# Optimization experiments

Measured on AMD Instinct MI355X. Metric: run time of the kernel, lower is better.

Reference implementation:

```python
import jax, jax.numpy as jnp
import numpy as np

PROP_TIME = 8  # matches init_kwargs prop_time


def _patches(x, dil):
    # x: [B,1,H,W] -> [B,9,H,W]; 'same' padding with the given dilation,
    # matching torch.nn.functional.unfold(kernel_size=3, dilation=dil, padding=dil).
    return jax.lax.conv_general_dilated_patches(
        x,
        filter_shape=(3, 3),
        window_strides=(1, 1),
        padding=[(dil, dil), (dil, dil)],
        rhs_dilation=(dil, dil),
    )


def setup_inputs() -> dict:
    key = jax.random.key(0)
    k1, k2, k3, k4 = jax.random.split(key, 4)
    B, H, W = 4, 352, 1216
    guided1 = jax.random.normal(k1, (B, 9, H, W), dtype=jnp.float32)
    guided2 = jax.random.normal(k2, (B, 9, H, W), dtype=jnp.float32)
    fuse = jax.random.uniform(k3, (B, 2, H, W), dtype=jnp.float32)
    x = jax.random.normal(k4, (B, 1, H, W), dtype=jnp.float32)
    return {"guided1": guided1, "guided2": guided2, "fuse": fuse, "x": x}


def reference(guided1, guided2, fuse, x):
    # softmax over the 9 kernel taps -> spatially varying normalized kernels
    kern1 = jax.nn.softmax(guided1, axis=1)  # [B,9,H,W]
    kern2 = jax.nn.softmax(guided2, axis=1)  # [B,9,H,W]
    f1 = fuse[:, 0:1]  # [B,1,H,W]
    f2 = fuse[:, 1:2]
    for _ in range(PROP_TIME):
        p1 = _patches(x, 1)  # [B,9,H,W]
        p2 = _patches(x, 2)
        o1 = jnp.sum(p1 * kern1, axis=1, keepdims=True)  # [B,1,H,W]
        o2 = jnp.sum(p2 * kern2, axis=1, keepdims=True)
        x = o1 * f1 + o2 * f2
    return x
```

## Files before the change

### kernel.cpp

```cpp
#include <hip/hip_runtime.h>

#define HH 352
#define WW 1216
#define NB 4
#define HWSZ (HH * WW)
#define WQ (WW / 4)
#define NQ (NB * HH * WQ)

typedef _Float16 half4 __attribute__((ext_vector_type(4)));
typedef _Float16 half8 __attribute__((ext_vector_type(8)));


__global__ __launch_bounds__(256, 4) void softmax_premul_kernel(
    const float* __restrict__ g1, const float* __restrict__ g2,
    const float* __restrict__ fuse, _Float16* __restrict__ ko) {
    int q = blockIdx.x * 256 + threadIdx.x;
    if (q >= NQ) return;
    int b   = q / (HH * WQ);
    int rem = q - b * (HH * WQ);
    long gbase = (long)b * 9 * HWSZ + (long)rem * 4;
    long fbase = (long)b * 2 * HWSZ + (long)rem * 4;

    float4 f1 = *(const float4*)(fuse + fbase);
    float4 f2 = *(const float4*)(fuse + fbase + HWSZ);

    half4 h1[9];
    {
        float e[9][4];
        float s0 = 0.f, s1 = 0.f, s2 = 0.f, s3 = 0.f;
#pragma unroll
        for (int k = 0; k < 9; k++) {
            float4 t = *(const float4*)(g1 + gbase + (long)k * HWSZ);
            e[k][0] = __expf(t.x); e[k][1] = __expf(t.y);
            e[k][2] = __expf(t.z); e[k][3] = __expf(t.w);
            s0 += e[k][0]; s1 += e[k][1]; s2 += e[k][2]; s3 += e[k][3];
        }
        float r0 = f1.x / s0, r1 = f1.y / s1, r2 = f1.z / s2, r3 = f1.w / s3;
#pragma unroll
        for (int k = 0; k < 9; k++) {
            h1[k][0] = (_Float16)(e[k][0] * r0);
            h1[k][1] = (_Float16)(e[k][1] * r1);
            h1[k][2] = (_Float16)(e[k][2] * r2);
            h1[k][3] = (_Float16)(e[k][3] * r3);
        }
    }
    {
        float e[9][4];
        float s0 = 0.f, s1 = 0.f, s2 = 0.f, s3 = 0.f;
#pragma unroll
        for (int k = 0; k < 9; k++) {
            float4 t = *(const float4*)(g2 + gbase + (long)k * HWSZ);
            e[k][0] = __expf(t.x); e[k][1] = __expf(t.y);
            e[k][2] = __expf(t.z); e[k][3] = __expf(t.w);
            s0 += e[k][0]; s1 += e[k][1]; s2 += e[k][2]; s3 += e[k][3];
        }
        float r0 = f2.x / s0, r1 = f2.y / s1, r2 = f2.z / s2, r3 = f2.w / s3;
        long obase = (long)b * 9 * HWSZ * 2 + (long)rem * 8;
#pragma unroll
        for (int k = 0; k < 9; k++) {
            half8 t;
            t[0] = h1[k][0]; t[1] = (_Float16)(e[k][0] * r0);
            t[2] = h1[k][1]; t[3] = (_Float16)(e[k][1] * r1);
            t[4] = h1[k][2]; t[5] = (_Float16)(e[k][2] * r2);
            t[6] = h1[k][3]; t[7] = (_Float16)(e[k][3] * r3);
            *(half8*)(ko + obase + (long)k * HWSZ * 2) = t;
        }
    }
}

#define TW 64
#define TH 4
#define LW (TW + 2)
#define LROWS (TH + 4)
#define LSTRIDE (LW * 4)
#define TILES_W ((WQ + TW - 1) / TW)
#define TILES_H (HH / TH)

__global__ __launch_bounds__(256, 4) void prop_kernel(
    const _Float16* __restrict__ kk,
    const float* __restrict__ xin, float* __restrict__ xout) {
    __shared__ float xs[LROWS][LSTRIDE];

    int tid = threadIdx.x;
    int bidx = blockIdx.x;
    int tX = bidx % TILES_W;
    int r1 = bidx / TILES_W;
    int tY = r1 % TILES_H;
    int b  = r1 / TILES_H;
    int q0 = tX * TW;
    int h0 = tY * TH;

    const float* xb = xin + (long)b * HWSZ;

#pragma unroll
    for (int i = tid; i < LROWS * LW; i += 256) {
        int row = i / LW;
        int qc  = i - row * LW;
        int h   = h0 - 2 + row;
        int qg  = q0 - 1 + qc;
        float4 v = make_float4(0.f, 0.f, 0.f, 0.f);
        if (h >= 0 && h < HH && qg >= 0 && qg < WQ)
            v = *(const float4*)(xb + (long)h * WW + qg * 4);
        *(float4*)&xs[row][qc * 4] = v;
    }
    __syncthreads();

    int tx = tid & (TW - 1);
    int ty = tid >> 6;
    int qa = q0 + tx;
    if (qa >= WQ) return;

    int h = h0 + ty;
    long p0 = (long)h * WW + qa * 4;
    long kbase = ((long)b * 9 * HWSZ + p0) * 2;

    half8 kv[9];
#pragma unroll
    for (int k = 0; k < 9; k++)
        kv[k] = *(const half8*)(kk + kbase + (long)k * HWSZ * 2);

    float rb[5][8];
#pragma unroll
    for (int r = 0; r < 5; r++) {
        const float* p = &xs[ty + r][4 * tx + 2];
        float2 a = *(const float2*)(p);
        float4 m = *(const float4*)(p + 2);
        float2 z = *(const float2*)(p + 6);
        rb[r][0] = a.x; rb[r][1] = a.y;
        rb[r][2] = m.x; rb[r][3] = m.y; rb[r][4] = m.z; rb[r][5] = m.w;
        rb[r][6] = z.x; rb[r][7] = z.y;
    }

    float o[4] = {0.f, 0.f, 0.f, 0.f};
#pragma unroll
    for (int ky = 0; ky < 3; ky++) {
#pragma unroll
        for (int kx = 0; kx < 3; kx++) {
            int k = ky * 3 + kx;
#pragma unroll
            for (int j = 0; j < 4; j++) {
                o[j] = fmaf((float)kv[k][2 * j],     rb[ky + 1][j + 1 + kx], o[j]);
                o[j] = fmaf((float)kv[k][2 * j + 1], rb[2 * ky][j + 2 * kx], o[j]);
            }
        }
    }

    float4 res = make_float4(o[0], o[1], o[2], o[3]);
    *(float4*)(xout + (long)b * HWSZ + p0) = res;
}

extern "C" void kernel_launch(void* const* d_in, const int* in_sizes, int n_in,
                              void* d_out, int out_size, void* d_ws, size_t ws_size,
                              hipStream_t stream) {
    const float* g1   = (const float*)d_in[0];
    const float* g2   = (const float*)d_in[1];
    const float* fuse = (const float*)d_in[2];
    const float* x    = (const float*)d_in[3];
    float* out = (float*)d_out;

    _Float16* kk = (_Float16*)d_ws;
    float* bufA  = (float*)(kk + (size_t)NB * 9 * HWSZ * 2);

    int sm_blocks = (NQ + 255) / 256;
    softmax_premul_kernel<<<sm_blocks, 256, 0, stream>>>(g1, g2, fuse, kk);

    int pr_blocks = NB * TILES_H * TILES_W;
    prop_kernel<<<pr_blocks, 256, 0, stream>>>(kk, x,    bufA);
    prop_kernel<<<pr_blocks, 256, 0, stream>>>(kk, bufA, out);
    prop_kernel<<<pr_blocks, 256, 0, stream>>>(kk, out,  bufA);
    prop_kernel<<<pr_blocks, 256, 0, stream>>>(kk, bufA, out);
    prop_kernel<<<pr_blocks, 256, 0, stream>>>(kk, out,  bufA);
    prop_kernel<<<pr_blocks, 256, 0, stream>>>(kk, bufA, out);
    prop_kernel<<<pr_blocks, 256, 0, stream>>>(kk, out,  bufA);
    prop_kernel<<<pr_blocks, 256, 0, stream>>>(kk, bufA, out);
}
```

Measured before the change: 266.4 us.

## Fuse two propagation steps per launch with halo recompute in shared memory

Each prop launch now performs two propagation iterations: it loads a wider x halo tile, computes the intermediate step over an extended region into shared memory, then computes the final step for the interior tile. This halves the number of launches and the global round-trips of x, at the cost of redundant halo computation and extra kernel-weight loads for halo pixels. The softmax kernel is also reorganized to issue all 18 loads up front, with a lower occupancy hint.

```diff
diff --git a/kernel.cpp b/kernel.cpp
--- a/kernel.cpp
+++ b/kernel.cpp
@@ -4,14 +4,13 @@
 #define WW 1216
 #define NB 4
 #define HWSZ (HH * WW)
-#define WQ (WW / 4)
+#define WQ 304
 #define NQ (NB * HH * WQ)
 
-typedef _Float16 half4 __attribute__((ext_vector_type(4)));
 typedef _Float16 half8 __attribute__((ext_vector_type(8)));
 
 
-__global__ __launch_bounds__(256, 4) void softmax_premul_kernel(
+__global__ __launch_bounds__(256, 2) void softmax_premul_kernel(
     const float* __restrict__ g1, const float* __restrict__ g2,
     const float* __restrict__ fuse, _Float16* __restrict__ ko) {
     int q = blockIdx.x * 256 + threadIdx.x;
@@ -21,132 +20,166 @@
     long gbase = (long)b * 9 * HWSZ + (long)rem * 4;
     long fbase = (long)b * 2 * HWSZ + (long)rem * 4;
 
+    float4 t[18];
+#pragma unroll
+    for (int k = 0; k < 9; k++) t[k]     = *(const float4*)(g1 + gbase + (long)k * HWSZ);
+#pragma unroll
+    for (int k = 0; k < 9; k++) t[9 + k] = *(const float4*)(g2 + gbase + (long)k * HWSZ);
     float4 f1 = *(const float4*)(fuse + fbase);
     float4 f2 = *(const float4*)(fuse + fbase + HWSZ);
 
-    half4 h1[9];
-    {
-        float e[9][4];
-        float s0 = 0.f, s1 = 0.f, s2 = 0.f, s3 = 0.f;
-#pragma unroll
-        for (int k = 0; k < 9; k++) {
-            float4 t = *(const float4*)(g1 + gbase + (long)k * HWSZ);
-            e[k][0] = __expf(t.x); e[k][1] = __expf(t.y);
-            e[k][2] = __expf(t.z); e[k][3] = __expf(t.w);
-            s0 += e[k][0]; s1 += e[k][1]; s2 += e[k][2]; s3 += e[k][3];
-        }
-        float r0 = f1.x / s0, r1 = f1.y / s1, r2 = f1.z / s2, r3 = f1.w / s3;
-#pragma unroll
-        for (int k = 0; k < 9; k++) {
-            h1[k][0] = (_Float16)(e[k][0] * r0);
-            h1[k][1] = (_Float16)(e[k][1] * r1);
-            h1[k][2] = (_Float16)(e[k][2] * r2);
-            h1[k][3] = (_Float16)(e[k][3] * r3);
-        }
-    }
-    {
-        float e[9][4];
-        float s0 = 0.f, s1 = 0.f, s2 = 0.f, s3 = 0.f;
-#pragma unroll
-        for (int k = 0; k < 9; k++) {
-            float4 t = *(const float4*)(g2 + gbase + (long)k * HWSZ);
-            e[k][0] = __expf(t.x); e[k][1] = __expf(t.y);
-            e[k][2] = __expf(t.z); e[k][3] = __expf(t.w);
-            s0 += e[k][0]; s1 += e[k][1]; s2 += e[k][2]; s3 += e[k][3];
-        }
-        float r0 = f2.x / s0, r1 = f2.y / s1, r2 = f2.z / s2, r3 = f2.w / s3;
-        long obase = (long)b * 9 * HWSZ * 2 + (long)rem * 8;
-#pragma unroll
-        for (int k = 0; k < 9; k++) {
-            half8 t;
-            t[0] = h1[k][0]; t[1] = (_Float16)(e[k][0] * r0);
-            t[2] = h1[k][1]; t[3] = (_Float16)(e[k][1] * r1);
-            t[4] = h1[k][2]; t[5] = (_Float16)(e[k][2] * r2);
-            t[6] = h1[k][3]; t[7] = (_Float16)(e[k][3] * r3);
-            *(half8*)(ko + obase + (long)k * HWSZ * 2) = t;
-        }
+    float s1[4] = {0.f, 0.f, 0.f, 0.f}, s2[4] = {0.f, 0.f, 0.f, 0.f};
+#pragma unroll
+    for (int k = 0; k < 9; k++) {
+        t[k].x = __expf(t[k].x); s1[0] += t[k].x;
+        t[k].y = __expf(t[k].y); s1[1] += t[k].y;
+        t[k].z = __expf(t[k].z); s1[2] += t[k].z;
+        t[k].w = __expf(t[k].w); s1[3] += t[k].w;
+    }
+#pragma unroll
+    for (int k = 9; k < 18; k++) {
+        t[k].x = __expf(t[k].x); s2[0] += t[k].x;
+        t[k].y = __expf(t[k].y); s2[1] += t[k].y;
+        t[k].z = __expf(t[k].z); s2[2] += t[k].z;
+        t[k].w = __expf(t[k].w); s2[3] += t[k].w;
+    }
+    float r1[4], r2[4];
+    r1[0] = f1.x / s1[0]; r1[1] = f1.y / s1[1]; r1[2] = f1.z / s1[2]; r1[3] = f1.w / s1[3];
+    r2[0] = f2.x / s2[0]; r2[1] = f2.y / s2[1]; r2[2] = f2.z / s2[2]; r2[3] = f2.w / s2[3];
+
+    long obase = ((long)b * 9 * HWSZ + (long)rem * 4) * 2;
+#pragma unroll
+    for (int k = 0; k < 9; k++) {
+        half8 o;
+        o[0] = (_Float16)(t[k].x * r1[0]); o[1] = (_Float16)(t[9 + k].x * r2[0]);
+        o[2] = (_Float16)(t[k].y * r1[1]); o[3] = (_Float16)(t[9 + k].y * r2[1]);
+        o[4] = (_Float16)(t[k].z * r1[2]); o[5] = (_Float16)(t[9 + k].z * r2[2]);
+        o[6] = (_Float16)(t[k].w * r1[3]); o[7] = (_Float16)(t[9 + k].w * r2[3]);
+        *(half8*)(ko + obase + (long)k * HWSZ * 2) = o;
     }
 }
 
-#define TW 64
-#define TH 4
-#define LW (TW + 2)
-#define LROWS (TH + 4)
-#define LSTRIDE (LW * 4)
-#define TILES_W ((WQ + TW - 1) / TW)
-#define TILES_H (HH / TH)
-
-__global__ __launch_bounds__(256, 4) void prop_kernel(
+#define CTH 8
+#define CTQ 76
+#define R1H 12
+#define R1Q 78
+#define X0H 16
+#define X0Q 80
+#define NREG (R1H * R1Q)
+
+__global__ __launch_bounds__(512, 2) void prop2_kernel(
     const _Float16* __restrict__ kk,
     const float* __restrict__ xin, float* __restrict__ xout) {
-    __shared__ float xs[LROWS][LSTRIDE];
-
-    int tid = threadIdx.x;
+    __shared__ float x0s[X0H][X0Q * 4];
+    __shared__ float x1s[R1H][R1Q * 4];
+
+    int tid  = threadIdx.x;
     int bidx = blockIdx.x;
-    int tX = bidx % TILES_W;
-    int r1 = bidx / TILES_W;
-    int tY = r1 % TILES_H;
-    int b  = r1 / TILES_H;
-    int q0 = tX * TW;
-    int h0 = tY * TH;
-
+    int tX = bidx & 3;
+    int rr = bidx >> 2;
+    int tY = rr % 44;
+    int b  = rr / 44;
+    int q0 = tX * CTQ;
+    int h0 = tY * CTH;
     const float* xb = xin + (long)b * HWSZ;
 
-#pragma unroll
-    for (int i = tid; i < LROWS * LW; i += 256) {
-        int row = i / LW;
-        int qc  = i - row * LW;
-        int h   = h0 - 2 + row;
-        int qg  = q0 - 1 + qc;
+    half8 kv[2][9];
+    int own_r[2], own_c[2];
+    bool own_v[2];
+#pragma unroll
+    for (int o = 0; o < 2; o++) {
+        int idx = tid + o * 512;
+        bool active = idx < NREG;
+        int r = idx / R1Q;
+        int c = idx - r * R1Q;
+        own_r[o] = r; own_c[o] = c;
+        int h  = h0 - 2 + r;
+        int qg = q0 - 1 + c;
+        bool valid = active && (h >= 0) && (h < HH) && (qg >= 0) && (qg < WQ);
+        own_v[o] = active;
+        long kb = ((long)b * 9 * HWSZ + (long)h * WW + qg * 4) * 2;
+#pragma unroll
+        for (int k = 0; k < 9; k++) {
+            half8 z = {};
+            kv[o][k] = valid ? *(const half8*)(kk + kb + (long)k * HWSZ * 2) : z;
+        }
+    }
+
+    for (int i = tid; i < X0H * X0Q; i += 512) {
+        int r = i / X0Q;
+        int c = i - r * X0Q;
+        int h  = h0 - 4 + r;
+        int qg = q0 - 2 + c;
         float4 v = make_float4(0.f, 0.f, 0.f, 0.f);
         if (h >= 0 && h < HH && qg >= 0 && qg < WQ)
             v = *(const float4*)(xb + (long)h * WW + qg * 4);
-        *(float4*)&xs[row][qc * 4] = v;
+        *(float4*)&x0s[r][c * 4] = v;
     }
     __syncthreads();
 
-    int tx = tid & (TW - 1);
-    int ty = tid >> 6;
-    int qa = q0 + tx;
-    if (qa >= WQ) return;
-
-    int h = h0 + ty;
-    long p0 = (long)h * WW + qa * 4;
-    long kbase = ((long)b * 9 * HWSZ + p0) * 2;
-
-    half8 kv[9];
-#pragma unroll
-    for (int k = 0; k < 9; k++)
-        kv[k] = *(const half8*)(kk + kbase + (long)k * HWSZ * 2);
-
-    float rb[5][8];
-#pragma unroll
-    for (int r = 0; r < 5; r++) {
-        const float* p = &xs[ty + r][4 * tx + 2];
-        float2 a = *(const float2*)(p);
-        float4 m = *(const float4*)(p + 2);
-        float2 z = *(const float2*)(p + 6);
-        rb[r][0] = a.x; rb[r][1] = a.y;
-        rb[r][2] = m.x; rb[r][3] = m.y; rb[r][4] = m.z; rb[r][5] = m.w;
-        rb[r][6] = z.x; rb[r][7] = z.y;
-    }
-
-    float o[4] = {0.f, 0.f, 0.f, 0.f};
-#pragma unroll
-    for (int ky = 0; ky < 3; ky++) {
-#pragma unroll
-        for (int kx = 0; kx < 3; kx++) {
-            int k = ky * 3 + kx;
-#pragma unroll
-            for (int j = 0; j < 4; j++) {
-                o[j] = fmaf((float)kv[k][2 * j],     rb[ky + 1][j + 1 + kx], o[j]);
-                o[j] = fmaf((float)kv[k][2 * j + 1], rb[2 * ky][j + 2 * kx], o[j]);
+#pragma unroll
+    for (int o = 0; o < 2; o++) {
+        if (!own_v[o]) continue;
+        int r = own_r[o], c = own_c[o];
+        float rb[5][8];
+#pragma unroll
+        for (int y = 0; y < 5; y++) {
+            const float* p = &x0s[r + y][4 * c + 2];
+            float2 a = *(const float2*)(p);
+            float4 m = *(const float4*)(p + 2);
+            float2 z = *(const float2*)(p + 6);
+            rb[y][0] = a.x; rb[y][1] = a.y;
+            rb[y][2] = m.x; rb[y][3] = m.y; rb[y][4] = m.z; rb[y][5] = m.w;
+            rb[y][6] = z.x; rb[y][7] = z.y;
+        }
+        float ov[4] = {0.f, 0.f, 0.f, 0.f};
+#pragma unroll
+        for (int ky = 0; ky < 3; ky++)
+#pragma unroll
+            for (int kx = 0; kx < 3; kx++) {
+                int k = ky * 3 + kx;
+#pragma unroll
+                for (int j = 0; j < 4; j++) {
+                    ov[j] = fmaf((float)kv[o][k][2 * j],     rb[ky + 1][j + 1 + kx], ov[j]);
+                    ov[j] = fmaf((float)kv[o][k][2 * j + 1], rb[2 * ky][j + 2 * kx], ov[j]);
+                }
             }
+        *(float4*)&x1s[r][c * 4] = make_float4(ov[0], ov[1], ov[2], ov[3]);
+    }
+    __syncthreads();
+
+#pragma unroll
+    for (int o = 0; o < 2; o++) {
+        int r = own_r[o], c = own_c[o];
+        if (!own_v[o] || r < 2 || r >= 10 || c < 1 || c >= 77) continue;
+        float rb[5][8];
+#pragma unroll
+        for (int y = 0; y < 5; y++) {
+            const float* p = &x1s[r - 2 + y][4 * c - 2];
+            float2 a = *(const float2*)(p);
+            float4 m = *(const float4*)(p + 2);
+            float2 z = *(const float2*)(p + 6);
+            rb[y][0] = a.x; rb[y][1] = a.y;
+            rb[y][2] = m.x; rb[y][3] = m.y; rb[y][4] = m.z; rb[y][5] = m.w;
+            rb[y][6] = z.x; rb[y][7] = z.y;
         }
-    }
-
-    float4 res = make_float4(o[0], o[1], o[2], o[3]);
-    *(float4*)(xout + (long)b * HWSZ + p0) = res;
+        float ov[4] = {0.f, 0.f, 0.f, 0.f};
+#pragma unroll
+        for (int ky = 0; ky < 3; ky++)
+#pragma unroll
+            for (int kx = 0; kx < 3; kx++) {
+                int k = ky * 3 + kx;
+#pragma unroll
+                for (int j = 0; j < 4; j++) {
+                    ov[j] = fmaf((float)kv[o][k][2 * j],     rb[ky + 1][j + 1 + kx], ov[j]);
+                    ov[j] = fmaf((float)kv[o][k][2 * j + 1], rb[2 * ky][j + 2 * kx], ov[j]);
+                }
+            }
+        int h  = h0 - 2 + r;
+        int qg = q0 - 1 + c;
+        *(float4*)(xout + (long)b * HWSZ + (long)h * WW + qg * 4) =
+            make_float4(ov[0], ov[1], ov[2], ov[3]);
+    }
 }
 
 extern "C" void kernel_launch(void* const* d_in, const int* in_sizes, int n_in,
@@ -164,13 +197,9 @@
     int sm_blocks = (NQ + 255) / 256;
     softmax_premul_kernel<<<sm_blocks, 256, 0, stream>>>(g1, g2, fuse, kk);
 
-    int pr_blocks = NB * TILES_H * TILES_W;
-    prop_kernel<<<pr_blocks, 256, 0, stream>>>(kk, x,    bufA);
-    prop_kernel<<<pr_blocks, 256, 0, stream>>>(kk, bufA, out);
-    prop_kernel<<<pr_blocks, 256, 0, stream>>>(kk, out,  bufA);
-    prop_kernel<<<pr_blocks, 256, 0, stream>>>(kk, bufA, out);
-    prop_kernel<<<pr_blocks, 256, 0, stream>>>(kk, out,  bufA);
-    prop_kernel<<<pr_blocks, 256, 0, stream>>>(kk, bufA, out);
-    prop_kernel<<<pr_blocks, 256, 0, stream>>>(kk, out,  bufA);
-    prop_kernel<<<pr_blocks, 256, 0, stream>>>(kk, bufA, out);
+    int pr_blocks = NB * 44 * 4;
+    prop2_kernel<<<pr_blocks, 512, 0, stream>>>(kk, x,    bufA);
+    prop2_kernel<<<pr_blocks, 512, 0, stream>>>(kk, bufA, out);
+    prop2_kernel<<<pr_blocks, 512, 0, stream>>>(kk, out,  bufA);
+    prop2_kernel<<<pr_blocks, 512, 0, stream>>>(kk, bufA, out);
 }
```

Measured after the change: 276.9 us. 1.04x slower.

## Fuse first propagation step into softmax kernel and store intermediates in fp16

Applied to the files above, without the earlier changes.

Folds the first propagation iteration into the softmax/premultiply kernel, which reads x directly from global memory and reuses the freshly computed kernel weights still held in registers. This removes one launch and one full pass over the fp16 kernel-weight buffer. Intermediate x buffers are also stored as fp16 rather than fp32, halving their read and write traffic; only the last step writes fp32. The trade-off is extra rounding error in x over the seven fp16 round trips, plus higher register pressure in the fused kernel.

```diff
diff --git a/kernel.cpp b/kernel.cpp
--- a/kernel.cpp
+++ b/kernel.cpp
@@ -4,82 +4,112 @@
 #define WW 1216
 #define NB 4
 #define HWSZ (HH * WW)
-#define WQ (WW / 4)
-#define NQ (NB * HH * WQ)
+#define WQ 304
+#define BHQ (HH * WQ)
+#define NQ (NB * BHQ)
 
 typedef _Float16 half4 __attribute__((ext_vector_type(4)));
 typedef _Float16 half8 __attribute__((ext_vector_type(8)));
 
 
-__global__ __launch_bounds__(256, 4) void softmax_premul_kernel(
+__global__ __launch_bounds__(256, 4) void softmax_prop1_kernel(
     const float* __restrict__ g1, const float* __restrict__ g2,
-    const float* __restrict__ fuse, _Float16* __restrict__ ko) {
+    const float* __restrict__ fuse, const float* __restrict__ x0,
+    _Float16* __restrict__ kk, _Float16* __restrict__ x1) {
     int q = blockIdx.x * 256 + threadIdx.x;
     if (q >= NQ) return;
-    int b   = q / (HH * WQ);
-    int rem = q - b * (HH * WQ);
+    int b   = q / BHQ;
+    int rem = q - b * BHQ;
+    int h   = rem / WQ;
+    int wq  = rem - h * WQ;
+    int w0  = wq * 4;
     long gbase = (long)b * 9 * HWSZ + (long)rem * 4;
     long fbase = (long)b * 2 * HWSZ + (long)rem * 4;
 
+    float4 t[18];
+#pragma unroll
+    for (int k = 0; k < 9; k++) t[k]     = *(const float4*)(g1 + gbase + (long)k * HWSZ);
+#pragma unroll
+    for (int k = 0; k < 9; k++) t[9 + k] = *(const float4*)(g2 + gbase + (long)k * HWSZ);
     float4 f1 = *(const float4*)(fuse + fbase);
     float4 f2 = *(const float4*)(fuse + fbase + HWSZ);
 
-    half4 h1[9];
-    {
-        float e[9][4];
-        float s0 = 0.f, s1 = 0.f, s2 = 0.f, s3 = 0.f;
-#pragma unroll
-        for (int k = 0; k < 9; k++) {
-            float4 t = *(const float4*)(g1 + gbase + (long)k * HWSZ);
-            e[k][0] = __expf(t.x); e[k][1] = __expf(t.y);
-            e[k][2] = __expf(t.z); e[k][3] = __expf(t.w);
-            s0 += e[k][0]; s1 += e[k][1]; s2 += e[k][2]; s3 += e[k][3];
+    float s1[4] = {0.f, 0.f, 0.f, 0.f}, s2[4] = {0.f, 0.f, 0.f, 0.f};
+#pragma unroll
+    for (int k = 0; k < 9; k++) {
+        t[k].x = __expf(t[k].x); s1[0] += t[k].x;
+        t[k].y = __expf(t[k].y); s1[1] += t[k].y;
+        t[k].z = __expf(t[k].z); s1[2] += t[k].z;
+        t[k].w = __expf(t[k].w); s1[3] += t[k].w;
+    }
+#pragma unroll
+    for (int k = 9; k < 18; k++) {
+        t[k].x = __expf(t[k].x); s2[0] += t[k].x;
+        t[k].y = __expf(t[k].y); s2[1] += t[k].y;
+        t[k].z = __expf(t[k].z); s2[2] += t[k].z;
+        t[k].w = __expf(t[k].w); s2[3] += t[k].w;
+    }
+    float r1[4], r2[4];
+    r1[0] = f1.x / s1[0]; r1[1] = f1.y / s1[1]; r1[2] = f1.z / s1[2]; r1[3] = f1.w / s1[3];
+    r2[0] = f2.x / s2[0]; r2[1] = f2.y / s2[1]; r2[2] = f2.z / s2[2]; r2[3] = f2.w / s2[3];
+
+    long obase = gbase * 2;
+    half8 kv[9];
+#pragma unroll
+    for (int k = 0; k < 9; k++) {
+        half8 o;
+        o[0] = (_Float16)(t[k].x * r1[0]); o[1] = (_Float16)(t[9 + k].x * r2[0]);
+        o[2] = (_Float16)(t[k].y * r1[1]); o[3] = (_Float16)(t[9 + k].y * r2[1]);
+        o[4] = (_Float16)(t[k].z * r1[2]); o[5] = (_Float16)(t[9 + k].z * r2[2]);
+        o[6] = (_Float16)(t[k].w * r1[3]); o[7] = (_Float16)(t[9 + k].w * r2[3]);
+        kv[k] = o;
+        *(half8*)(kk + obase + (long)k * HWSZ * 2) = o;
+    }
+
+    const float* xb = x0 + (long)b * HWSZ;
+    float rb[5][8];
+#pragma unroll
+    for (int r = 0; r < 5; r++) {
+        int hh = h - 2 + r;
+        bool rv = (hh >= 0) && (hh < HH);
+        const float* rp = xb + (long)hh * WW;
+        float4 mid = rv ? *(const float4*)(rp + w0) : make_float4(0.f, 0.f, 0.f, 0.f);
+        float2 lft = (rv && w0 > 0) ? *(const float2*)(rp + w0 - 2) : make_float2(0.f, 0.f);
+        float2 rgt = (rv && (w0 + 5) < WW) ? *(const float2*)(rp + w0 + 4) : make_float2(0.f, 0.f);
+        rb[r][0] = lft.x; rb[r][1] = lft.y;
+        rb[r][2] = mid.x; rb[r][3] = mid.y; rb[r][4] = mid.z; rb[r][5] = mid.w;
+        rb[r][6] = rgt.x; rb[r][7] = rgt.y;
+    }
+    float o[4] = {0.f, 0.f, 0.f, 0.f};
+#pragma unroll
+    for (int ky = 0; ky < 3; ky++)
+#pragma unroll
+        for (int kx = 0; kx < 3; kx++) {
+            int k = ky * 3 + kx;
+#pragma unroll
+            for (int j = 0; j < 4; j++) {
+                o[j] = fmaf((float)kv[k][2 * j],     rb[ky + 1][j + 1 + kx], o[j]);
+                o[j] = fmaf((float)kv[k][2 * j + 1], rb[2 * ky][j + 2 * kx], o[j]);
+            }
         }
-        float r0 = f1.x / s0, r1 = f1.y / s1, r2 = f1.z / s2, r3 = f1.w / s3;
-#pragma unroll
-        for (int k = 0; k < 9; k++) {
-            h1[k][0] = (_Float16)(e[k][0] * r0);
-            h1[k][1] = (_Float16)(e[k][1] * r1);
-            h1[k][2] = (_Float16)(e[k][2] * r2);
-            h1[k][3] = (_Float16)(e[k][3] * r3);
-        }
-    }
-    {
-        float e[9][4];
-        float s0 = 0.f, s1 = 0.f, s2 = 0.f, s3 = 0.f;
-#pragma unroll
-        for (int k = 0; k < 9; k++) {
-            float4 t = *(const float4*)(g2 + gbase + (long)k * HWSZ);
-            e[k][0] = __expf(t.x); e[k][1] = __expf(t.y);
-            e[k][2] = __expf(t.z); e[k][3] = __expf(t.w);
-            s0 += e[k][0]; s1 += e[k][1]; s2 += e[k][2]; s3 += e[k][3];
-        }
-        float r0 = f2.x / s0, r1 = f2.y / s1, r2 = f2.z / s2, r3 = f2.w / s3;
-        long obase = (long)b * 9 * HWSZ * 2 + (long)rem * 8;
-#pragma unroll
-        for (int k = 0; k < 9; k++) {
-            half8 t;
-            t[0] = h1[k][0]; t[1] = (_Float16)(e[k][0] * r0);
-            t[2] = h1[k][1]; t[3] = (_Float16)(e[k][1] * r1);
-            t[4] = h1[k][2]; t[5] = (_Float16)(e[k][2] * r2);
-            t[6] = h1[k][3]; t[7] = (_Float16)(e[k][3] * r3);
-            *(half8*)(ko + obase + (long)k * HWSZ * 2) = t;
-        }
-    }
+    half4 xo;
+    xo[0] = (_Float16)o[0]; xo[1] = (_Float16)o[1];
+    xo[2] = (_Float16)o[2]; xo[3] = (_Float16)o[3];
+    *(half4*)(x1 + (long)b * HWSZ + (long)rem * 4) = xo;
 }
 
 #define TW 64
 #define TH 4
 #define LW (TW + 2)
 #define LROWS (TH + 4)
-#define LSTRIDE (LW * 4)
-#define TILES_W ((WQ + TW - 1) / TW)
+#define TILES_W 5
 #define TILES_H (HH / TH)
 
+template <int OUT16>
 __global__ __launch_bounds__(256, 4) void prop_kernel(
     const _Float16* __restrict__ kk,
-    const float* __restrict__ xin, float* __restrict__ xout) {
-    __shared__ float xs[LROWS][LSTRIDE];
+    const _Float16* __restrict__ xin, void* __restrict__ xout_) {
+    __shared__ float xs[LROWS][LW * 4];
 
     int tid = threadIdx.x;
     int bidx = blockIdx.x;
@@ -90,7 +120,7 @@
     int q0 = tX * TW;
     int h0 = tY * TH;
 
-    const float* xb = xin + (long)b * HWSZ;
+    const _Float16* xb = xin + (long)b * HWSZ;
 
 #pragma unroll
     for (int i = tid; i < LROWS * LW; i += 256) {
@@ -99,8 +129,10 @@
         int h   = h0 - 2 + row;
         int qg  = q0 - 1 + qc;
         float4 v = make_float4(0.f, 0.f, 0.f, 0.f);
-        if (h >= 0 && h < HH && qg >= 0 && qg < WQ)
-            v = *(const float4*)(xb + (long)h * WW + qg * 4);
+        if (h >= 0 && h < HH && qg >= 0 && qg < WQ) {
+            half4 hv = *(const half4*)(xb + (long)h * WW + qg * 4);
+            v = make_float4((float)hv[0], (float)hv[1], (float)hv[2], (float)hv[3]);
+        }
         *(float4*)&xs[row][qc * 4] = v;
     }
     __syncthreads();
@@ -133,7 +165,7 @@
 
     float o[4] = {0.f, 0.f, 0.f, 0.f};
 #pragma unroll
-    for (int ky = 0; ky < 3; ky++) {
+    for (int ky = 0; ky < 3; ky++)
 #pragma unroll
         for (int kx = 0; kx < 3; kx++) {
             int k = ky * 3 + kx;
@@ -143,10 +175,16 @@
                 o[j] = fmaf((float)kv[k][2 * j + 1], rb[2 * ky][j + 2 * kx], o[j]);
             }
         }
-    }
-
-    float4 res = make_float4(o[0], o[1], o[2], o[3]);
-    *(float4*)(xout + (long)b * HWSZ + p0) = res;
+
+    if (OUT16) {
+        half4 xo;
+        xo[0] = (_Float16)o[0]; xo[1] = (_Float16)o[1];
+        xo[2] = (_Float16)o[2]; xo[3] = (_Float16)o[3];
+        *(half4*)((_Float16*)xout_ + (long)b * HWSZ + p0) = xo;
+    } else {
+        *(float4*)((float*)xout_ + (long)b * HWSZ + p0) =
+            make_float4(o[0], o[1], o[2], o[3]);
+    }
 }
 
 extern "C" void kernel_launch(void* const* d_in, const int* in_sizes, int n_in,
@@ -158,19 +196,19 @@
     const float* x    = (const float*)d_in[3];
     float* out = (float*)d_out;
 
-    _Float16* kk = (_Float16*)d_ws;
-    float* bufA  = (float*)(kk + (size_t)NB * 9 * HWSZ * 2);
+    _Float16* kk   = (_Float16*)d_ws;
+    _Float16* bufA = kk + (size_t)NB * 9 * HWSZ * 2;
+    _Float16* bufB = bufA + (size_t)NB * HWSZ;
 
     int sm_blocks = (NQ + 255) / 256;
-    softmax_premul_kernel<<<sm_blocks, 256, 0, stream>>>(g1, g2, fuse, kk);
+    softmax_prop1_kernel<<<sm_blocks, 256, 0, stream>>>(g1, g2, fuse, x, kk, bufA);
 
     int pr_blocks = NB * TILES_H * TILES_W;
-    prop_kernel<<<pr_blocks, 256, 0, stream>>>(kk, x,    bufA);
-    prop_kernel<<<pr_blocks, 256, 0, stream>>>(kk, bufA, out);
-    prop_kernel<<<pr_blocks, 256, 0, stream>>>(kk, out,  bufA);
-    prop_kernel<<<pr_blocks, 256, 0, stream>>>(kk, bufA, out);
-    prop_kernel<<<pr_blocks, 256, 0, stream>>>(kk, out,  bufA);
-    prop_kernel<<<pr_blocks, 256, 0, stream>>>(kk, bufA, out);
-    prop_kernel<<<pr_blocks, 256, 0, stream>>>(kk, out,  bufA);
-    prop_kernel<<<pr_blocks, 256, 0, stream>>>(kk, bufA, out);
+    prop_kernel<1><<<pr_blocks, 256, 0, stream>>>(kk, bufA, bufB);
+    prop_kernel<1><<<pr_blocks, 256, 0, stream>>>(kk, bufB, bufA);
+    prop_kernel<1><<<pr_blocks, 256, 0, stream>>>(kk, bufA, bufB);
+    prop_kernel<1><<<pr_blocks, 256, 0, stream>>>(kk, bufB, bufA);
+    prop_kernel<1><<<pr_blocks, 256, 0, stream>>>(kk, bufA, bufB);
+    prop_kernel<1><<<pr_blocks, 256, 0, stream>>>(kk, bufB, bufA);
+    prop_kernel<0><<<pr_blocks, 256, 0, stream>>>(kk, bufA, out);
 }
```

Result: faster. 246.5 us (-7.5%).
